# Kernel optimization log

Measured on AMD Instinct MI355X. Metric: run time of the kernel, lower is better.

The kernel has to match this reference:

```python
import jax, jax.numpy as jnp
import numpy as np


def setup_inputs() -> dict:
    key = jax.random.key(0)
    k1, k2, k3 = jax.random.split(key, 3)
    B, C, Q, E = 32, 2048, 128, 200
    x_contexts = jax.random.normal(k1, (B, C, E), dtype=jnp.float32)
    x_questions = jax.random.normal(k2, (B, Q, E), dtype=jnp.float32)
    # weight of nn.Linear(3E, 1, bias=False), flattened to (3E,)
    w_sim = jax.random.normal(k3, (3 * E,), dtype=jnp.float32) * (1.0 / np.sqrt(3 * E))
    return {"x_contexts": x_contexts, "x_questions": x_questions, "w_sim": w_sim}


def reference(x_contexts, x_questions, w_sim):
    # x_contexts: [B,C,E], x_questions: [B,Q,E], w_sim: [3E]
    E = x_contexts.shape[-1]
    w1, w2, w3 = w_sim[:E], w_sim[E:2 * E], w_sim[2 * E:]
    # Trilinear similarity S[b,c,q] = w1.c + w2.q + w3.(c*q), decomposed so the
    # [B,C,Q,3E] tensor of the original expand+cat+linear is never materialized.
    s_c = jnp.einsum('bce,e->bc', x_contexts, w1)              # [B,C]
    s_q = jnp.einsum('bqe,e->bq', x_questions, w2)             # [B,Q]
    s_cq = jnp.einsum('bce,bqe->bcq', x_contexts * w3, x_questions)  # [B,C,Q]
    S = s_cq + s_c[:, :, None] + s_q[:, None, :]               # [B,C,Q]

    # Context-to-question: row softmax over Q, then attend over questions.
    c2q = jnp.einsum('bcq,bqe->bce', jax.nn.softmax(S, axis=-1), x_questions)

    # Question-to-context: max over Q, softmax over C, attend over contexts.
    q2c_w = jax.nn.softmax(jnp.max(S, axis=-1), axis=-1)       # [B,C]
    q2c = jnp.einsum('bc,bce->be', q2c_w, x_contexts)          # [B,E]
    q2c = q2c[:, None, :]                                      # broadcast to [B,C,E]

    return jnp.concatenate(
        [x_contexts, c2q, x_contexts * c2q, x_contexts * q2c], axis=-1)  # [B,C,4E]
```

## Files before the change

kernel.cpp:

```cpp
#include <hip/hip_runtime.h>

#define B_ 32
#define C_ 2048
#define Q_ 128
#define E_ 200
#define TB 32

typedef __attribute__((ext_vector_type(4))) float f32x4;

__global__ __launch_bounds__(256) void xqt_kernel(const float* __restrict__ xq,
                                                  float* __restrict__ xqT) {
    const int idx = blockIdx.x * 256 + threadIdx.x;
    const int q  = idx & (Q_ - 1);
    const int be = idx >> 7;
    const int b  = be / E_;
    const int e  = be - b * E_;
    xqT[idx] = xq[((size_t)b * Q_ + q) * E_ + e];
}

__global__ __launch_bounds__(128) void sq_kernel(const float* __restrict__ xqT,
                                                 const float* __restrict__ w,
                                                 float* __restrict__ sq) {
    const int b = blockIdx.x, q = threadIdx.x;
    const float* base = xqT + (size_t)b * E_ * Q_ + q;
    float a = 0.f;
    for (int e = 0; e < E_; ++e) a = fmaf(base[e * Q_], w[E_ + e], a);
    sq[b * Q_ + q] = a;
}

__global__ __launch_bounds__(256) void row2_kernel(const float* __restrict__ xc_g,
                                                   const float* __restrict__ xq_g,
                                                   const float* __restrict__ xqT_g,
                                                   const float* __restrict__ w_g,
                                                   const float* __restrict__ sq_g,
                                                   float* __restrict__ m_g,
                                                   float* __restrict__ out) {
    __shared__ float scw3_l[TB][E_];
    __shared__ float P_l[TB][Q_];
    __shared__ float sc_l[TB];

    const int t    = threadIdx.x;
    const int b    = blockIdx.x >> 6;
    const int tile = blockIdx.x & 63;
    const int bc0  = b * C_ + tile * TB;

    {
        const int r  = t >> 3;
        const int k  = t & 7;
        const int e0 = k * 25;
        const float* xc_row = xc_g + (size_t)(bc0 + r) * E_;
        float p1 = 0.f;
        #pragma unroll
        for (int i = 0; i < 25; ++i) {
            const int e = e0 + i;
            const float v = xc_row[e];
            scw3_l[r][e] = v * w_g[2 * E_ + e];
            p1 = fmaf(v, w_g[e], p1);
        }
        p1 += __shfl_xor(p1, 1);
        p1 += __shfl_xor(p1, 2);
        p1 += __shfl_xor(p1, 4);
        if (k == 0) sc_l[r] = p1;
    }
    __syncthreads();

    const int qg = t & 31;
    const int cg = t >> 5;
    const int c4 = cg * 4;
    const int q4 = qg * 4;

    f32x4 acc[4] = {};
    const float* xqT_b = xqT_g + (size_t)b * E_ * Q_;
    for (int e = 0; e < E_; e += 4) {
        const f32x4 x0 = *(const f32x4*)&xqT_b[(e + 0) * Q_ + q4];
        const f32x4 x1 = *(const f32x4*)&xqT_b[(e + 1) * Q_ + q4];
        const f32x4 x2 = *(const f32x4*)&xqT_b[(e + 2) * Q_ + q4];
        const f32x4 x3 = *(const f32x4*)&xqT_b[(e + 3) * Q_ + q4];
        #pragma unroll
        for (int ci = 0; ci < 4; ++ci) {
            const f32x4 a = *(const f32x4*)&scw3_l[c4 + ci][e];
            acc[ci] += a.x * x0 + a.y * x1 + a.z * x2 + a.w * x3;
        }
    }

    const f32x4 sqv = *(const f32x4*)&sq_g[b * Q_ + q4];
    float mx[4], sm[4];
    #pragma unroll
    for (int ci = 0; ci < 4; ++ci) {
        acc[ci] += sc_l[c4 + ci] + sqv;
        mx[ci] = fmaxf(fmaxf(acc[ci].x, acc[ci].y), fmaxf(acc[ci].z, acc[ci].w));
    }
    #pragma unroll
    for (int off = 16; off; off >>= 1) {
        #pragma unroll
        for (int ci = 0; ci < 4; ++ci) mx[ci] = fmaxf(mx[ci], __shfl_xor(mx[ci], off));
    }
    if (qg == 0) {
        #pragma unroll
        for (int ci = 0; ci < 4; ++ci) m_g[bc0 + c4 + ci] = mx[ci];
    }
    #pragma unroll
    for (int ci = 0; ci < 4; ++ci) {
        f32x4 p;
        p.x = __expf(acc[ci].x - mx[ci]);
        p.y = __expf(acc[ci].y - mx[ci]);
        p.z = __expf(acc[ci].z - mx[ci]);
        p.w = __expf(acc[ci].w - mx[ci]);
        acc[ci] = p;
        sm[ci] = (p.x + p.y) + (p.z + p.w);
    }
    #pragma unroll
    for (int off = 16; off; off >>= 1) {
        #pragma unroll
        for (int ci = 0; ci < 4; ++ci) sm[ci] += __shfl_xor(sm[ci], off);
    }
    #pragma unroll
    for (int ci = 0; ci < 4; ++ci) {
        acc[ci] *= (1.f / sm[ci]);
        *(f32x4*)&P_l[c4 + ci][q4] = acc[ci];
    }
    __syncthreads();

    const float* xq_b = xq_g + (size_t)b * Q_ * E_;
    #pragma unroll
    for (int pass = 0; pass < 2; ++pass) {
        const int e4 = pass * 128 + q4;
        if (e4 < E_) {
            f32x4 o[4] = {};
            for (int q = 0; q < Q_; q += 4) {
                const f32x4 xv0 = *(const f32x4*)&xq_b[(q + 0) * E_ + e4];
                const f32x4 xv1 = *(const f32x4*)&xq_b[(q + 1) * E_ + e4];
                const f32x4 xv2 = *(const f32x4*)&xq_b[(q + 2) * E_ + e4];
                const f32x4 xv3 = *(const f32x4*)&xq_b[(q + 3) * E_ + e4];
                #pragma unroll
                for (int ci = 0; ci < 4; ++ci) {
                    const f32x4 p = *(const f32x4*)&P_l[c4 + ci][q];
                    o[ci] += p.x * xv0 + p.y * xv1 + p.z * xv2 + p.w * xv3;
                }
            }
            #pragma unroll
            for (int ci = 0; ci < 4; ++ci) {
                const size_t row = (size_t)(bc0 + c4 + ci);
                const f32x4 xcv = *(const f32x4*)&xc_g[row * E_ + e4];
                float* orow = out + row * (4 * E_);
                *(f32x4*)&orow[e4]          = xcv;
                *(f32x4*)&orow[E_ + e4]     = o[ci];
                *(f32x4*)&orow[2 * E_ + e4] = xcv * o[ci];
            }
        }
    }
}

__global__ __launch_bounds__(256) void stats_kernel(const float* __restrict__ m_g,
                                                    float* __restrict__ bstat) {
    __shared__ float red[4];
    const int b = blockIdx.x, t = threadIdx.x;
    float mx = -3.4e38f;
    for (int c = t; c < C_; c += 256) mx = fmaxf(mx, m_g[b * C_ + c]);
    #pragma unroll
    for (int off = 32; off; off >>= 1) mx = fmaxf(mx, __shfl_xor(mx, off));
    if ((t & 63) == 0) red[t >> 6] = mx;
    __syncthreads();
    mx = fmaxf(fmaxf(red[0], red[1]), fmaxf(red[2], red[3]));
    __syncthreads();
    float sum = 0.f;
    for (int c = t; c < C_; c += 256) sum += __expf(m_g[b * C_ + c] - mx);
    #pragma unroll
    for (int off = 32; off; off >>= 1) sum += __shfl_xor(sum, off);
    if ((t & 63) == 0) red[t >> 6] = sum;
    __syncthreads();
    if (t == 0) {
        bstat[b]      = mx;
        bstat[B_ + b] = red[0] + red[1] + red[2] + red[3];
    }
}

__global__ __launch_bounds__(256) void q2c_partial(const float* __restrict__ xc_g,
                                                   const float* __restrict__ m_g,
                                                   const float* __restrict__ bstat,
                                                   float* __restrict__ part) {
    __shared__ float wl[128];
    const int blk = blockIdx.x;
    const int b = blk >> 4, g = blk & 15;
    const int t = threadIdx.x;
    const float mx  = bstat[b];
    const float inv = 1.f / bstat[B_ + b];
    if (t < 128) wl[t] = __expf(m_g[b * C_ + g * 128 + t] - mx) * inv;
    __syncthreads();
    if (t < E_) {
        float acc = 0.f;
        const float* base = xc_g + ((size_t)(b * C_ + g * 128)) * E_ + t;
        for (int c = 0; c < 128; ++c) acc = fmaf(wl[c], base[(size_t)c * E_], acc);
        part[(size_t)blk * E_ + t] = acc;
    }
}

__global__ __launch_bounds__(256) void q2c_reduce(const float* __restrict__ part,
                                                  float* __restrict__ q2c) {
    const int b = blockIdx.x, t = threadIdx.x;
    if (t < E_) {
        float a = 0.f;
        #pragma unroll
        for (int g = 0; g < 16; ++g) a += part[(size_t)(b * 16 + g) * E_ + t];
        q2c[b * E_ + t] = a;
    }
}

__global__ __launch_bounds__(256) void out4_kernel(const float* __restrict__ xc_g,
                                                   const float* __restrict__ q2c,
                                                   float* __restrict__ out) {
    const unsigned int idx = blockIdx.x * 256u + threadIdx.x;
    const unsigned int e = idx % E_;
    const unsigned int row = idx / E_;
    const unsigned int b = row / C_;
    const float v = xc_g[idx] * q2c[b * E_ + e];
    out[(size_t)row * (4 * E_) + 3 * E_ + e] = v;
}

extern "C" void kernel_launch(void* const* d_in, const int* in_sizes, int n_in,
                              void* d_out, int out_size, void* d_ws, size_t ws_size,
                              hipStream_t stream) {
    const float* xc = (const float*)d_in[0];
    const float* xq = (const float*)d_in[1];
    const float* w  = (const float*)d_in[2];
    for (int i = 0; i < n_in; ++i) {
        if      (in_sizes[i] == B_ * C_ * E_) xc = (const float*)d_in[i];
        else if (in_sizes[i] == B_ * Q_ * E_) xq = (const float*)d_in[i];
        else if (in_sizes[i] == 3 * E_)       w  = (const float*)d_in[i];
    }
    float* out = (float*)d_out;

    float* ws    = (float*)d_ws;
    float* sq    = ws;
    float* m     = sq + B_ * Q_;
    float* bstat = m + B_ * C_;
    float* q2c   = bstat + 2 * B_;
    float* xqT   = q2c + B_ * E_;
    float* part  = xqT;

    xqt_kernel  <<<(B_ * E_ * Q_) / 256, 256, 0, stream>>>(xq, xqT);
    sq_kernel   <<<B_,              128, 0, stream>>>(xqT, w, sq);
    row2_kernel <<<B_ * (C_ / TB),  256, 0, stream>>>(xc, xq, xqT, w, sq, m, out);
    stats_kernel<<<B_,              256, 0, stream>>>(m, bstat);
    q2c_partial <<<B_ * 16,         256, 0, stream>>>(xc, m, bstat, part);
    q2c_reduce  <<<B_,              256, 0, stream>>>(part, q2c);
    out4_kernel <<<(B_ * C_ * E_) / 256, 256, 0, stream>>>(xc, q2c, out);
}
```

Baseline: 426.8 us.

## Tile transpose via LDS, reuse LDS buffer, remap blocks for XCD locality, vectorize out4

Several changes land at once. The xq transpose now goes through a padded 32x33 shared tile so both its reads and writes are coalesced. row2_kernel reuses a single LDS buffer for the scaled contexts and for the softmax probabilities, which needs an extra barrier, and its block index is remapped so each group of 8 consecutive blocks (likely one per XCD on this part) covers a different set of batches, improving L2 locality. q2c_partial gets the same batch remap, out4_kernel writes float4 vectors, and a few unroll pragmas are added. The smaller LDS footprint may raise occupancy, at the cost of one more sync per block.

```diff
diff --git a/kernel.cpp b/kernel.cpp
--- a/kernel.cpp
+++ b/kernel.cpp
@@ -10,12 +10,24 @@
 
 __global__ __launch_bounds__(256) void xqt_kernel(const float* __restrict__ xq,
                                                   float* __restrict__ xqT) {
-    const int idx = blockIdx.x * 256 + threadIdx.x;
-    const int q  = idx & (Q_ - 1);
-    const int be = idx >> 7;
-    const int b  = be / E_;
-    const int e  = be - b * E_;
-    xqT[idx] = xq[((size_t)b * Q_ + q) * E_ + e];
+    __shared__ float tl[32][33];
+    const int blk = blockIdx.x;
+    const int b  = blk / 28;
+    const int r  = blk - b * 28;
+    const int qt = r / 7, et = r - (r / 7) * 7;
+    const int q0 = qt * 32, e0 = et * 32;
+    const int tx = threadIdx.x & 31, ty = threadIdx.x >> 5;
+    #pragma unroll
+    for (int i = 0; i < 4; ++i) {
+        const int q = q0 + ty + 8 * i, e = e0 + tx;
+        if (e < E_) tl[ty + 8 * i][tx] = xq[((size_t)b * Q_ + q) * E_ + e];
+    }
+    __syncthreads();
+    #pragma unroll
+    for (int i = 0; i < 4; ++i) {
+        const int e = e0 + ty + 8 * i, q = q0 + tx;
+        if (e < E_) xqT[((size_t)b * E_ + e) * Q_ + q] = tl[tx][ty + 8 * i];
+    }
 }
 
 __global__ __launch_bounds__(128) void sq_kernel(const float* __restrict__ xqT,
@@ -24,6 +36,7 @@
     const int b = blockIdx.x, q = threadIdx.x;
     const float* base = xqT + (size_t)b * E_ * Q_ + q;
     float a = 0.f;
+    #pragma unroll 8
     for (int e = 0; e < E_; ++e) a = fmaf(base[e * Q_], w[E_ + e], a);
     sq[b * Q_ + q] = a;
 }
@@ -35,14 +48,16 @@
                                                    const float* __restrict__ sq_g,
                                                    float* __restrict__ m_g,
                                                    float* __restrict__ out) {
-    __shared__ float scw3_l[TB][E_];
-    __shared__ float P_l[TB][Q_];
+    __shared__ float buf[TB][E_];
     __shared__ float sc_l[TB];
 
-    const int t    = threadIdx.x;
-    const int b    = blockIdx.x >> 6;
-    const int tile = blockIdx.x & 63;
-    const int bc0  = b * C_ + tile * TB;
+    const int t = threadIdx.x;
+    const int blk = blockIdx.x;
+    const int x   = blk & 7;
+    const int g   = blk >> 3;
+    const int b   = x * 4 + (g >> 6);
+    const int tile = g & 63;
+    const int bc0 = b * C_ + tile * TB;
 
     {
         const int r  = t >> 3;
@@ -54,7 +69,7 @@
         for (int i = 0; i < 25; ++i) {
             const int e = e0 + i;
             const float v = xc_row[e];
-            scw3_l[r][e] = v * w_g[2 * E_ + e];
+            buf[r][e] = v * w_g[2 * E_ + e];
             p1 = fmaf(v, w_g[e], p1);
         }
         p1 += __shfl_xor(p1, 1);
@@ -71,6 +86,7 @@
 
     f32x4 acc[4] = {};
     const float* xqT_b = xqT_g + (size_t)b * E_ * Q_;
+    #pragma unroll 2
     for (int e = 0; e < E_; e += 4) {
         const f32x4 x0 = *(const f32x4*)&xqT_b[(e + 0) * Q_ + q4];
         const f32x4 x1 = *(const f32x4*)&xqT_b[(e + 1) * Q_ + q4];
@@ -78,10 +94,11 @@
         const f32x4 x3 = *(const f32x4*)&xqT_b[(e + 3) * Q_ + q4];
         #pragma unroll
         for (int ci = 0; ci < 4; ++ci) {
-            const f32x4 a = *(const f32x4*)&scw3_l[c4 + ci][e];
+            const f32x4 a = *(const f32x4*)&buf[c4 + ci][e];
             acc[ci] += a.x * x0 + a.y * x1 + a.z * x2 + a.w * x3;
         }
     }
+    __syncthreads();
 
     const f32x4 sqv = *(const f32x4*)&sq_g[b * Q_ + q4];
     float mx[4], sm[4];
@@ -117,7 +134,7 @@
     #pragma unroll
     for (int ci = 0; ci < 4; ++ci) {
         acc[ci] *= (1.f / sm[ci]);
-        *(f32x4*)&P_l[c4 + ci][q4] = acc[ci];
+        *(f32x4*)&buf[c4 + ci][q4] = acc[ci];
     }
     __syncthreads();
 
@@ -134,7 +151,7 @@
                 const f32x4 xv3 = *(const f32x4*)&xq_b[(q + 3) * E_ + e4];
                 #pragma unroll
                 for (int ci = 0; ci < 4; ++ci) {
-                    const f32x4 p = *(const f32x4*)&P_l[c4 + ci][q];
+                    const f32x4 p = *(const f32x4*)&buf[c4 + ci][q];
                     o[ci] += p.x * xv0 + p.y * xv1 + p.z * xv2 + p.w * xv3;
                 }
             }
@@ -181,7 +198,8 @@
                                                    float* __restrict__ part) {
     __shared__ float wl[128];
     const int blk = blockIdx.x;
-    const int b = blk >> 4, g = blk & 15;
+    const int x = blk & 7, u = blk >> 3;
+    const int b = x * 4 + (u >> 4), g = u & 15;
     const int t = threadIdx.x;
     const float mx  = bstat[b];
     const float inv = 1.f / bstat[B_ + b];
@@ -190,8 +208,9 @@
     if (t < E_) {
         float acc = 0.f;
         const float* base = xc_g + ((size_t)(b * C_ + g * 128)) * E_ + t;
+        #pragma unroll 8
         for (int c = 0; c < 128; ++c) acc = fmaf(wl[c], base[(size_t)c * E_], acc);
-        part[(size_t)blk * E_ + t] = acc;
+        part[(size_t)(b * 16 + g) * E_ + t] = acc;
     }
 }
 
@@ -210,11 +229,13 @@
                                                    const float* __restrict__ q2c,
                                                    float* __restrict__ out) {
     const unsigned int idx = blockIdx.x * 256u + threadIdx.x;
-    const unsigned int e = idx % E_;
-    const unsigned int row = idx / E_;
+    const unsigned int n = idx * 4u;
+    const unsigned int e = n % E_;
+    const unsigned int row = n / E_;
     const unsigned int b = row / C_;
-    const float v = xc_g[idx] * q2c[b * E_ + e];
-    out[(size_t)row * (4 * E_) + 3 * E_ + e] = v;
+    const f32x4 xcv = *(const f32x4*)&xc_g[n];
+    const f32x4 qv  = *(const f32x4*)&q2c[b * E_ + e];
+    *(f32x4*)&out[(size_t)row * (4 * E_) + 3 * E_ + e] = xcv * qv;
 }
 
 extern "C" void kernel_launch(void* const* d_in, const int* in_sizes, int n_in,
@@ -238,11 +259,11 @@
     float* xqT   = q2c + B_ * E_;
     float* part  = xqT;
 
-    xqt_kernel  <<<(B_ * E_ * Q_) / 256, 256, 0, stream>>>(xq, xqT);
+    xqt_kernel  <<<B_ * 28,         256, 0, stream>>>(xq, xqT);
     sq_kernel   <<<B_,              128, 0, stream>>>(xqT, w, sq);
     row2_kernel <<<B_ * (C_ / TB),  256, 0, stream>>>(xc, xq, xqT, w, sq, m, out);
     stats_kernel<<<B_,              256, 0, stream>>>(m, bstat);
     q2c_partial <<<B_ * 16,         256, 0, stream>>>(xc, m, bstat, part);
     q2c_reduce  <<<B_,              256, 0, stream>>>(part, q2c);
-    out4_kernel <<<(B_ * C_ * E_) / 256, 256, 0, stream>>>(xc, q2c, out);
-}
+    out4_kernel <<<(B_ * C_ * E_ / 4) / 256, 256, 0, stream>>>(xc, q2c, out);
+}
```

After: 455.3 us. +6.7%, slower.
